# Kernel optimization log

Hardware: AMD Instinct MI355X
Metric: run time of the kernel (lower is better)

The kernel has to match this reference:

```python
import jax, jax.numpy as jnp
import numpy as np
import math

B, H, S, D = 2, 16, 2048, 64

def setup_inputs() -> dict:
    key = jax.random.key(0)
    kq, kk, kv = jax.random.split(key, 3)
    return {
        "q": jax.random.normal(kq, (B, H, S, D), dtype=jnp.float32),
        "k": jax.random.normal(kk, (B, H, S, D), dtype=jnp.float32),
        "v": jax.random.normal(kv, (B, H, S, D), dtype=jnp.float32),
        "temp": jnp.ones((1,), dtype=jnp.float32),
    }

def reference(q, k, v, temp):
    dk = q.shape[-1]
    # scores: [B,H,S,S] = q @ k^T / (temp * sqrt(dk))
    scores = jnp.einsum("bhsd,bhtd->bhst", q, k) / (temp[0] * math.sqrt(dk))
    attention = jax.nn.softmax(scores, axis=-1)
    y = jnp.einsum("bhst,bhtd->bhsd", attention, v)
    return y
```

## Files before the change

### kernel.cpp

```cpp
#include <hip/hip_runtime.h>
#include <stdint.h>


typedef _Float16 f16;
typedef __attribute__((ext_vector_type(4))) _Float16 f16x4;
typedef __attribute__((ext_vector_type(8))) _Float16 f16x8;
typedef __attribute__((ext_vector_type(4))) float f32x4;

constexpr int Bc = 2, Hc = 16, Sc = 2048, Dc = 64;
constexpr size_t NE = (size_t)Bc * Hc * Sc * Dc;

__device__ inline void gld_lds16(const f16* g, f16* l) {
  __builtin_amdgcn_global_load_lds(
      (const __attribute__((address_space(1))) unsigned int*)g,
      (__attribute__((address_space(3))) unsigned int*)l, 16, 0, 0);
}

__global__ __launch_bounds__(256)
void prep(const float* __restrict__ kp, const float* __restrict__ vp,
          const float* __restrict__ temp,
          f16* __restrict__ kh, f16* __restrict__ vt) {
  const int tid = threadIdx.x;
  const int bh = blockIdx.x & 31;
  const int st = blockIdx.x >> 5;
  const float ksc = 1.44269504088896340736f / (temp[0] * 8.0f);

  const size_t base = (size_t)bh * Sc * Dc + (size_t)st * 64 * Dc;
  const float* kg = kp + base;
  f16* khg = kh + base;
#pragma unroll
  for (int i = 0; i < 4; ++i) {
    int f = tid + (i << 8);
    f32x4 a = *(const f32x4*)(kg + f * 4);
    *(f16x4*)(khg + f * 4) = (f16x4){(f16)(a.x * ksc), (f16)(a.y * ksc),
                                     (f16)(a.z * ksc), (f16)(a.w * ksc)};
  }
  const int sb = tid & 15, db = tid >> 4;
  const float* vg = vp + base;
  f32x4 r0 = *(const f32x4*)(vg + (4 * sb + 0) * Dc + 4 * db);
  f32x4 r1 = *(const f32x4*)(vg + (4 * sb + 1) * Dc + 4 * db);
  f32x4 r2 = *(const f32x4*)(vg + (4 * sb + 2) * Dc + 4 * db);
  f32x4 r3 = *(const f32x4*)(vg + (4 * sb + 3) * Dc + 4 * db);
  f16* vtg = vt + (size_t)bh * Dc * Sc + (size_t)st * 64 + 4 * sb;
  *(f16x4*)(vtg + (size_t)(4 * db + 0) * Sc) = (f16x4){(f16)r0.x, (f16)r1.x, (f16)r2.x, (f16)r3.x};
  *(f16x4*)(vtg + (size_t)(4 * db + 1) * Sc) = (f16x4){(f16)r0.y, (f16)r1.y, (f16)r2.y, (f16)r3.y};
  *(f16x4*)(vtg + (size_t)(4 * db + 2) * Sc) = (f16x4){(f16)r0.z, (f16)r1.z, (f16)r2.z, (f16)r3.z};
  *(f16x4*)(vtg + (size_t)(4 * db + 3) * Sc) = (f16x4){(f16)r0.w, (f16)r1.w, (f16)r2.w, (f16)r3.w};
}

__global__ __launch_bounds__(256, 3)
void fa8(const float* __restrict__ qp, const f16* __restrict__ kh,
         const f16* __restrict__ vt, float* __restrict__ out) {
  __shared__ __align__(16) char smem[34816];
  __shared__ float Lred[4][64];
  f16* Kb = (f16*)smem;
  f16* Vb = (f16*)(smem + 16384);
  float* OsA = (float*)smem;
  float* OsB = (float*)(smem + 16896);

  const int tid = threadIdx.x, lane = tid & 63, w = tid >> 6;
  const int lq = lane & 15, qd = lane >> 4;
  const int L = blockIdx.x;
  const int bh = L & 31;
  const int qt = L >> 5;

  const size_t base = (size_t)bh * Sc * Dc;

  const int jk = 2 * w;
  const int r0s = 8 * jk + (lane >> 3);
  const int r1s = r0s + 8;
  const int oct = (lane & 7) ^ ((lane >> 3) & 7);
  const f16* kg0 = kh + base + r0s * 64 + oct * 8;
  const f16* kg1 = kh + base + r1s * 64 + oct * 8;
  const f16* vg0 = vt + (size_t)bh * Dc * Sc + (size_t)r0s * Sc + oct * 8;
  const f16* vg1 = vt + (size_t)bh * Dc * Sc + (size_t)r1s * Sc + oct * 8;

  auto stage = [&](int kt) {
    int b = kt & 1;
    gld_lds16(kg0 + kt * 4096, Kb + b * 4096 + jk * 512);
    gld_lds16(kg1 + kt * 4096, Kb + b * 4096 + (jk + 1) * 512);
    gld_lds16(vg0 + kt * 64, Vb + b * 4096 + jk * 512);
    gld_lds16(vg1 + kt * 64, Vb + b * 4096 + (jk + 1) * 512);
  };

  const int kfr = 16 * w + lq;
  const int koff0 = kfr * 64 + ((qd) ^ (lq & 7)) * 8;
  const int koff1 = kfr * 64 + (((4 + qd)) ^ (lq & 7)) * 8;
  const int vsl = (2 * w + (qd >> 1)) ^ (lq & 7);
  int voff[4];
#pragma unroll
  for (int dt = 0; dt < 4; ++dt)
    voff[dt] = (16 * dt + lq) * 64 + vsl * 8 + (qd & 1) * 4;

  const float* qg = qp + base + (size_t)qt * 64 * Dc;
  f16x8 Qf[4][2];
#pragma unroll
  for (int nt = 0; nt < 4; ++nt)
#pragma unroll
    for (int kc = 0; kc < 2; ++kc) {
      const float* p = qg + (16 * nt + lq) * Dc + 32 * kc + 8 * qd;
      f32x4 a = *(const f32x4*)p;
      f32x4 b = *(const f32x4*)(p + 4);
      auto p0 = __builtin_amdgcn_cvt_pkrtz(a.x, a.y);
      auto p1 = __builtin_amdgcn_cvt_pkrtz(a.z, a.w);
      auto p2 = __builtin_amdgcn_cvt_pkrtz(b.x, b.y);
      auto p3 = __builtin_amdgcn_cvt_pkrtz(b.z, b.w);
      f16x8 qf;
      ((decltype(p0)*)&qf)[0] = p0;
      ((decltype(p0)*)&qf)[1] = p1;
      ((decltype(p0)*)&qf)[2] = p2;
      ((decltype(p0)*)&qf)[3] = p3;
      Qf[nt][kc] = qf;
    }

  f32x4 Oa[4][4];
  float ls[4];
#pragma unroll
  for (int nt = 0; nt < 4; ++nt) {
    ls[nt] = 0.f;
#pragma unroll
    for (int dt = 0; dt < 4; ++dt) Oa[nt][dt] = (f32x4){0.f, 0.f, 0.f, 0.f};
  }

  stage(0);

#pragma unroll 1
  for (int kt = 0; kt < 32; ++kt) {
    __syncthreads();
    if (kt + 1 < 32) stage(kt + 1);

    const f16* KB = Kb + (kt & 1) * 4096;
    const f16* VB = Vb + (kt & 1) * 4096;
    f16x8 K0 = *(const f16x8*)(KB + koff0);
    f16x8 K1 = *(const f16x8*)(KB + koff1);

    f32x4 St[4];
#pragma unroll
    for (int nt = 0; nt < 4; ++nt) {
      f32x4 a = (f32x4){0.f, 0.f, 0.f, 0.f};
      a = __builtin_amdgcn_mfma_f32_16x16x32_f16(K0, Qf[nt][0], a, 0, 0, 0);
      a = __builtin_amdgcn_mfma_f32_16x16x32_f16(K1, Qf[nt][1], a, 0, 0, 0);
      St[nt] = a;
    }

    f16x4 Vf[4];
#pragma unroll
    for (int dt = 0; dt < 4; ++dt) Vf[dt] = *(const f16x4*)(VB + voff[dt]);

    f16x4 Pf[4];
#pragma unroll
    for (int nt = 0; nt < 4; ++nt) {
      float e0 = exp2f(St[nt].x), e1 = exp2f(St[nt].y);
      float e2 = exp2f(St[nt].z), e3 = exp2f(St[nt].w);
      ls[nt] += (e0 + e1) + (e2 + e3);
      auto lo = __builtin_amdgcn_cvt_pkrtz(e0, e1);
      auto hi = __builtin_amdgcn_cvt_pkrtz(e2, e3);
      f16x4 p;
      ((decltype(lo)*)&p)[0] = lo;
      ((decltype(lo)*)&p)[1] = hi;
      Pf[nt] = p;
    }

#pragma unroll
    for (int nt = 0; nt < 4; ++nt)
#pragma unroll
      for (int dt = 0; dt < 4; ++dt)
        Oa[nt][dt] = __builtin_amdgcn_mfma_f32_16x16x16f16(Pf[nt], Vf[dt],
                                                           Oa[nt][dt], 0, 0, 0);
  }

#pragma unroll
  for (int nt = 0; nt < 4; ++nt) {
    float l = ls[nt];
    l += __shfl_xor(l, 16, 64);
    l += __shfl_xor(l, 32, 64);
    ls[nt] = l;
  }
  __syncthreads();
  if (qd == 0) {
#pragma unroll
    for (int nt = 0; nt < 4; ++nt) Lred[w][16 * nt + lq] = ls[nt];
  }
  float* Os = (w & 2) ? OsB : OsA;
  if (!(w & 1)) {
#pragma unroll
    for (int nt = 0; nt < 4; ++nt)
#pragma unroll
      for (int dt = 0; dt < 4; ++dt)
#pragma unroll
        for (int r = 0; r < 4; ++r)
          Os[(16 * nt + 4 * qd + r) * 66 + 16 * dt + lq] = Oa[nt][dt][r];
  }
  __syncthreads();
  if (w & 1) {
#pragma unroll
    for (int nt = 0; nt < 4; ++nt)
#pragma unroll
      for (int dt = 0; dt < 4; ++dt)
#pragma unroll
        for (int r = 0; r < 4; ++r)
          Os[(16 * nt + 4 * qd + r) * 66 + 16 * dt + lq] += Oa[nt][dt][r];
  }
  __syncthreads();

  float* og = out + base + (size_t)qt * 64 * Dc;
#pragma unroll
  for (int r = 0; r < 16; ++r) {
    int row = 16 * w + r;
    float l = Lred[0][row] + Lred[1][row] + Lred[2][row] + Lred[3][row];
    float vo = OsA[row * 66 + lane] + OsB[row * 66 + lane];
    og[(size_t)row * Dc + lane] = vo / l;
  }
}

extern "C" void kernel_launch(void* const* d_in, const int* in_sizes, int n_in,
                              void* d_out, int out_size, void* d_ws, size_t ws_size,
                              hipStream_t stream) {
  const float* q    = (const float*)d_in[0];
  const float* k    = (const float*)d_in[1];
  const float* v    = (const float*)d_in[2];
  const float* temp = (const float*)d_in[3];
  float* out = (float*)d_out;

  f16* kh = (f16*)d_ws;
  f16* vt = kh + NE;

  prep<<<dim3(Bc * Hc * (Sc / 64)), dim3(256), 0, stream>>>(k, v, temp, kh, vt);
  fa8<<<dim3(Bc * Hc * (Sc / 64)), dim3(256), 0, stream>>>(q, kh, vt, out);
}
```

Baseline: 163.4 us.

## Give each wave private LDS K/V slices and drop per-tile block barriers

Each wave now loads its own 16-key slice of K and V into a private LDS region, so the per-iteration __syncthreads is replaced by explicit vmcnt/lgkmcnt waits. The loop is unrolled by two with double buffering and the next stage is issued right after the LDS reads. Other changes: raw exp2 intrinsics, a register-pinned zero accumulator, and launch bounds raised to 4 blocks per CU. These aim to cut barrier stalls and raise occupancy, at the cost of relying on hand-written waitcnt correctness and a tighter register budget.

```diff
diff --git a/kernel.cpp b/kernel.cpp
--- a/kernel.cpp
+++ b/kernel.cpp
@@ -48,15 +48,11 @@
   *(f16x4*)(vtg + (size_t)(4 * db + 3) * Sc) = (f16x4){(f16)r0.w, (f16)r1.w, (f16)r2.w, (f16)r3.w};
 }
 
-__global__ __launch_bounds__(256, 3)
-void fa8(const float* __restrict__ qp, const f16* __restrict__ kh,
+__global__ __launch_bounds__(256, 4)
+void fa9(const float* __restrict__ qp, const f16* __restrict__ kh,
          const f16* __restrict__ vt, float* __restrict__ out) {
-  __shared__ __align__(16) char smem[34816];
+  __shared__ __align__(16) char smem[33792];
   __shared__ float Lred[4][64];
-  f16* Kb = (f16*)smem;
-  f16* Vb = (f16*)(smem + 16384);
-  float* OsA = (float*)smem;
-  float* OsB = (float*)(smem + 16896);
 
   const int tid = threadIdx.x, lane = tid & 63, w = tid >> 6;
   const int lq = lane & 15, qd = lane >> 4;
@@ -66,31 +62,31 @@
 
   const size_t base = (size_t)bh * Sc * Dc;
 
-  const int jk = 2 * w;
-  const int r0s = 8 * jk + (lane >> 3);
-  const int r1s = r0s + 8;
+  f16* Kw = (f16*)smem + w * 2048;
+  f16* Vw = (f16*)(smem + 16384) + w * 2048;
+
   const int oct = (lane & 7) ^ ((lane >> 3) & 7);
-  const f16* kg0 = kh + base + r0s * 64 + oct * 8;
-  const f16* kg1 = kh + base + r1s * 64 + oct * 8;
-  const f16* vg0 = vt + (size_t)bh * Dc * Sc + (size_t)r0s * Sc + oct * 8;
-  const f16* vg1 = vt + (size_t)bh * Dc * Sc + (size_t)r1s * Sc + oct * 8;
-
-  auto stage = [&](int kt) {
-    int b = kt & 1;
-    gld_lds16(kg0 + kt * 4096, Kb + b * 4096 + jk * 512);
-    gld_lds16(kg1 + kt * 4096, Kb + b * 4096 + (jk + 1) * 512);
-    gld_lds16(vg0 + kt * 64, Vb + b * 4096 + jk * 512);
-    gld_lds16(vg1 + kt * 64, Vb + b * 4096 + (jk + 1) * 512);
+  const f16* kg0 = kh + base + (size_t)(16 * w + (lane >> 3)) * 64 + oct * 8;
+  const f16* kg1 = kg0 + 8 * 64;
+  const int vd = lane >> 1;
+  const int vc = (lane & 1) ^ ((lane >> 3) & 1);
+  const f16* vg0 = vt + (size_t)bh * Dc * Sc + (size_t)vd * Sc + 16 * w + vc * 8;
+  const f16* vg1 = vg0 + (size_t)32 * Sc;
+
+  auto stage = [&](int kt, int b) {
+    gld_lds16(kg0 + (size_t)kt * 4096, Kw + b * 1024);
+    gld_lds16(kg1 + (size_t)kt * 4096, Kw + b * 1024 + 512);
+    gld_lds16(vg0 + kt * 64, Vw + b * 1024);
+    gld_lds16(vg1 + kt * 64, Vw + b * 1024 + 512);
   };
 
-  const int kfr = 16 * w + lq;
-  const int koff0 = kfr * 64 + ((qd) ^ (lq & 7)) * 8;
-  const int koff1 = kfr * 64 + (((4 + qd)) ^ (lq & 7)) * 8;
-  const int vsl = (2 * w + (qd >> 1)) ^ (lq & 7);
+  const int koff0 = lq * 64 + ((qd) ^ (lq & 7)) * 8;
+  const int koff1 = lq * 64 + ((4 + qd) ^ (lq & 7)) * 8;
   int voff[4];
 #pragma unroll
   for (int dt = 0; dt < 4; ++dt)
-    voff[dt] = (16 * dt + lq) * 64 + vsl * 8 + (qd & 1) * 4;
+    voff[dt] = (16 * dt + lq) * 16 + (((qd >> 1) ^ ((lq >> 2) & 1)) << 3) +
+               (qd & 1) * 4;
 
   const float* qg = qp + base + (size_t)qt * 64 * Dc;
   f16x8 Qf[4][2];
@@ -113,6 +109,10 @@
       Qf[nt][kc] = qf;
     }
 
+  float z0 = 0.f, z1 = 0.f, z2 = 0.f, z3 = 0.f;
+  asm volatile("" : "+v"(z0), "+v"(z1), "+v"(z2), "+v"(z3));
+  const f32x4 Zc = (f32x4){z0, z1, z2, z3};
+
   f32x4 Oa[4][4];
   float ls[4];
 #pragma unroll
@@ -122,52 +122,60 @@
     for (int dt = 0; dt < 4; ++dt) Oa[nt][dt] = (f32x4){0.f, 0.f, 0.f, 0.f};
   }
 
-  stage(0);
+  stage(0, 0);
+  stage(1, 1);
+
+#define FA_BODY(BUF, WN, STGKT)                                               \
+  {                                                                           \
+    asm volatile("s_waitcnt vmcnt(" WN ")" ::: "memory");                     \
+    const f16* KB = Kw + (BUF) * 1024;                                        \
+    const f16* VB = Vw + (BUF) * 1024;                                        \
+    f16x8 K0 = *(const f16x8*)(KB + koff0);                                   \
+    f16x8 K1 = *(const f16x8*)(KB + koff1);                                   \
+    f16x4 Vf[4];                                                              \
+    _Pragma("unroll")                                                         \
+    for (int dt = 0; dt < 4; ++dt) Vf[dt] = *(const f16x4*)(VB + voff[dt]);   \
+    asm volatile("s_waitcnt lgkmcnt(0)" ::: "memory");                        \
+    if ((STGKT) < 32) stage((STGKT), (BUF));                                  \
+    f32x4 St[4];                                                              \
+    _Pragma("unroll")                                                         \
+    for (int nt = 0; nt < 4; ++nt) {                                          \
+      f32x4 a = __builtin_amdgcn_mfma_f32_16x16x32_f16(K0, Qf[nt][0], Zc, 0, 0, 0); \
+      a = __builtin_amdgcn_mfma_f32_16x16x32_f16(K1, Qf[nt][1], a, 0, 0, 0);  \
+      St[nt] = a;                                                             \
+    }                                                                         \
+    f16x4 Pf[4];                                                              \
+    _Pragma("unroll")                                                         \
+    for (int nt = 0; nt < 4; ++nt) {                                          \
+      float e0 = __builtin_amdgcn_exp2f(St[nt].x);                            \
+      float e1 = __builtin_amdgcn_exp2f(St[nt].y);                            \
+      float e2 = __builtin_amdgcn_exp2f(St[nt].z);                            \
+      float e3 = __builtin_amdgcn_exp2f(St[nt].w);                            \
+      ls[nt] += (e0 + e1) + (e2 + e3);                                        \
+      auto lo = __builtin_amdgcn_cvt_pkrtz(e0, e1);                           \
+      auto hi = __builtin_amdgcn_cvt_pkrtz(e2, e3);                           \
+      f16x4 p;                                                                \
+      ((decltype(lo)*)&p)[0] = lo;                                            \
+      ((decltype(lo)*)&p)[1] = hi;                                            \
+      Pf[nt] = p;                                                             \
+    }                                                                         \
+    _Pragma("unroll")                                                         \
+    for (int nt = 0; nt < 4; ++nt)                                            \
+      _Pragma("unroll")                                                       \
+      for (int dt = 0; dt < 4; ++dt)                                          \
+        Oa[nt][dt] = __builtin_amdgcn_mfma_f32_16x16x16f16(Pf[nt], Vf[dt],    \
+                                                           Oa[nt][dt], 0, 0, 0); \
+  }
 
 #pragma unroll 1
-  for (int kt = 0; kt < 32; ++kt) {
-    __syncthreads();
-    if (kt + 1 < 32) stage(kt + 1);
-
-    const f16* KB = Kb + (kt & 1) * 4096;
-    const f16* VB = Vb + (kt & 1) * 4096;
-    f16x8 K0 = *(const f16x8*)(KB + koff0);
-    f16x8 K1 = *(const f16x8*)(KB + koff1);
-
-    f32x4 St[4];
-#pragma unroll
-    for (int nt = 0; nt < 4; ++nt) {
-      f32x4 a = (f32x4){0.f, 0.f, 0.f, 0.f};
-      a = __builtin_amdgcn_mfma_f32_16x16x32_f16(K0, Qf[nt][0], a, 0, 0, 0);
-      a = __builtin_amdgcn_mfma_f32_16x16x32_f16(K1, Qf[nt][1], a, 0, 0, 0);
-      St[nt] = a;
-    }
-
-    f16x4 Vf[4];
-#pragma unroll
-    for (int dt = 0; dt < 4; ++dt) Vf[dt] = *(const f16x4*)(VB + voff[dt]);
-
-    f16x4 Pf[4];
-#pragma unroll
-    for (int nt = 0; nt < 4; ++nt) {
-      float e0 = exp2f(St[nt].x), e1 = exp2f(St[nt].y);
-      float e2 = exp2f(St[nt].z), e3 = exp2f(St[nt].w);
-      ls[nt] += (e0 + e1) + (e2 + e3);
-      auto lo = __builtin_amdgcn_cvt_pkrtz(e0, e1);
-      auto hi = __builtin_amdgcn_cvt_pkrtz(e2, e3);
-      f16x4 p;
-      ((decltype(lo)*)&p)[0] = lo;
-      ((decltype(lo)*)&p)[1] = hi;
-      Pf[nt] = p;
-    }
-
-#pragma unroll
-    for (int nt = 0; nt < 4; ++nt)
-#pragma unroll
-      for (int dt = 0; dt < 4; ++dt)
-        Oa[nt][dt] = __builtin_amdgcn_mfma_f32_16x16x16f16(Pf[nt], Vf[dt],
-                                                           Oa[nt][dt], 0, 0, 0);
-  }
+  for (int kt2 = 0; kt2 < 15; ++kt2) {
+    FA_BODY(0, "4", 2 * kt2 + 2)
+    FA_BODY(1, "4", 2 * kt2 + 3)
+  }
+  FA_BODY(0, "4", 32)
+  FA_BODY(1, "0", 32)
+
+#undef FA_BODY
 
 #pragma unroll
   for (int nt = 0; nt < 4; ++nt) {
@@ -181,6 +189,8 @@
 #pragma unroll
     for (int nt = 0; nt < 4; ++nt) Lred[w][16 * nt + lq] = ls[nt];
   }
+  float* OsA = (float*)smem;
+  float* OsB = (float*)(smem + 16896);
   float* Os = (w & 2) ? OsB : OsA;
   if (!(w & 1)) {
 #pragma unroll
@@ -226,5 +236,5 @@
   f16* vt = kh + NE;
 
   prep<<<dim3(Bc * Hc * (Sc / 64)), dim3(256), 0, stream>>>(k, v, temp, kh, vt);
-  fa8<<<dim3(Bc * Hc * (Sc / 64)), dim3(256), 0, stream>>>(q, kh, vt, out);
-}
+  fa9<<<dim3(Bc * Hc * (Sc / 64)), dim3(256), 0, stream>>>(q, kh, vt, out);
+}
```

New measurement: 316.7 us. 93.8% more time.
